# Kernel optimization log

Hardware: AMD Instinct MI355X
Metric: run time of the kernel (lower is better)

The kernel has to match this reference:

```python
import jax, jax.numpy as jnp
import numpy as np

DIM = 1536
NUM_HEADS = 12
HEAD_DIM = DIM // NUM_HEADS  # 128
EPS = 1e-6


def _rms_norm(x, weight, eps=EPS):
    # x: [B, S, C], computed in float32 like the torch module
    xf = x.astype(jnp.float32)
    xf = xf * jax.lax.rsqrt(jnp.mean(xf * xf, axis=-1, keepdims=True) + eps)
    return (xf * weight).astype(x.dtype)


def _rotate_half(x):
    x1, x2 = jnp.split(x, 2, axis=-1)
    return jnp.concatenate([-x2, x1], axis=-1)


def setup_inputs() -> dict:
    key = jax.random.key(0)
    ks = jax.random.split(key, 12)
    B, S = 1, 4096
    scale = 1.0 / np.sqrt(DIM)
    x = jax.random.normal(ks[0], (B, S, DIM), dtype=jnp.float32)
    # RoPE tables [S, head_dim]
    pos = jnp.arange(S, dtype=jnp.float32)[:, None]
    inv_freq = 1.0 / (10000.0 ** (jnp.arange(0, HEAD_DIM, 2, dtype=jnp.float32) / HEAD_DIM))
    ang = pos * inv_freq[None, :]                      # [S, head_dim/2]
    ang = jnp.concatenate([ang, ang], axis=-1)         # [S, head_dim]
    freqs_cos = jnp.cos(ang)
    freqs_sin = jnp.sin(ang)
    Wq = jax.random.normal(ks[1], (DIM, DIM), dtype=jnp.float32) * scale
    bq = jnp.zeros((DIM,), dtype=jnp.float32)
    Wk = jax.random.normal(ks[2], (DIM, DIM), dtype=jnp.float32) * scale
    bk = jnp.zeros((DIM,), dtype=jnp.float32)
    Wv = jax.random.normal(ks[3], (DIM, DIM), dtype=jnp.float32) * scale
    bv = jnp.zeros((DIM,), dtype=jnp.float32)
    Wo = jax.random.normal(ks[4], (DIM, DIM), dtype=jnp.float32) * scale
    bo = jnp.zeros((DIM,), dtype=jnp.float32)
    gq = jnp.ones((DIM,), dtype=jnp.float32)
    gk = jnp.ones((DIM,), dtype=jnp.float32)
    return {"x": x, "freqs_cos": freqs_cos, "freqs_sin": freqs_sin,
            "Wq": Wq, "bq": bq, "Wk": Wk, "bk": bk, "Wv": Wv, "bv": bv,
            "Wo": Wo, "bo": bo, "gq": gq, "gk": gk}


def reference(x, freqs_cos, freqs_sin, Wq, bq, Wk, bk, Wv, bv, Wo, bo, gq, gk):
    b, s, _ = x.shape
    n, d = NUM_HEADS, HEAD_DIM
    q = _rms_norm(x @ Wq.T + bq, gq).reshape(b, s, n, d)
    k = _rms_norm(x @ Wk.T + bk, gk).reshape(b, s, n, d)
    v = (x @ Wv.T + bv).reshape(b, s, n, d)
    # RoPE: freqs [S, d] -> broadcast over batch and heads
    cos = freqs_cos[None, :, None, :]
    sin = freqs_sin[None, :, None, :]
    q = q * cos + _rotate_half(q) * sin
    k = k * cos + _rotate_half(k) * sin
    # SDPA, non-causal
    scores = jnp.einsum('bqnd,bknd->bnqk', q, k) / jnp.sqrt(jnp.asarray(d, x.dtype))
    attn = jax.nn.softmax(scores, axis=-1)
    out = jnp.einsum('bnqk,bknd->bqnd', attn, v).reshape(b, s, n * d)
    return out @ Wo.T + bo
```

## Files before the change

### kernel.cpp

```cpp
#include <hip/hip_runtime.h>

typedef unsigned short ushort_t;
typedef short bf16x8 __attribute__((ext_vector_type(8)));
typedef float f32x4 __attribute__((ext_vector_type(4)));
typedef float f32x16 __attribute__((ext_vector_type(16)));

#define S_LEN 4096
#define DIM   1536
#define NH    12
#define HD    128

__device__ __forceinline__ float bf2f(ushort_t h) {
  union { unsigned u; float f; } v; v.u = ((unsigned)h) << 16; return v.f;
}
__device__ __forceinline__ ushort_t f2bf(float f) {
  union { float f; unsigned u; } v; v.f = f;
  return (ushort_t)((v.u + 0x7FFFu + ((v.u >> 16) & 1u)) >> 16);
}
__device__ __forceinline__ unsigned cvtpk(float lo, float hi_) {
  unsigned r; asm("v_cvt_pk_bf16_f32 %0, %1, %2" : "=v"(r) : "v"(lo), "v"(hi_)); return r;
}

#define GLD16(gp, lp) __builtin_amdgcn_global_load_lds( \
    (const __attribute__((address_space(1))) unsigned int*)(gp), \
    (__attribute__((address_space(3))) unsigned int*)(lp), 16, 0, 0)

__global__ void __launch_bounds__(256) cvt_bf16(const float* __restrict__ in,
                                                ushort_t* __restrict__ out, int n4) {
  int i = blockIdx.x * 256 + threadIdx.x;
  int stride = gridDim.x * 256;
  for (; i < n4; i += stride) {
    float4 v = ((const float4*)in)[i];
    ushort4 o;
    o.x = f2bf(v.x); o.y = f2bf(v.y); o.z = f2bf(v.z); o.w = f2bf(v.w);
    ((ushort4*)out)[i] = o;
  }
}

template <int F32OUT>
__global__ void __launch_bounds__(256) gemm_bt(
    const ushort_t* __restrict__ A, const ushort_t* __restrict__ Wbase,
    const float* __restrict__ b0, const float* __restrict__ b1, const float* __restrict__ b2,
    void* __restrict__ Cbase_v, int M, int N, int K)
{
  const int z = blockIdx.z;
  const ushort_t* W = Wbase + (size_t)z * N * K;
  const float* bias = (z == 0) ? b0 : (z == 1) ? b1 : b2;

  const int n0 = blockIdx.x * 128;
  const int m0 = blockIdx.y * 128;
  const int t = threadIdx.x;
  const int lane = t & 63;
  const int w = t >> 6;
  const int wr = w >> 1, wc = w & 1;
  const int mp = lane & 15, g = lane >> 4;

  __shared__ __attribute__((aligned(16))) ushort_t As[128 * 64];
  __shared__ __attribute__((aligned(16))) ushort_t Bs[128 * 64];

  f32x4 acc[4][4];
  f32x4 zero = {0.f, 0.f, 0.f, 0.f};
#pragma unroll
  for (int i = 0; i < 4; ++i)
#pragma unroll
    for (int j = 0; j < 4; ++j) acc[i][j] = zero;

  for (int kt = 0; kt < K; kt += 64) {
    __syncthreads();
#pragma unroll
    for (int i = 0; i < 4; ++i) {
      int p = i * 256 + t;
      int r = p >> 3, sl = p & 7;
      int sg = sl ^ (r & 7);
      GLD16(A + (size_t)(m0 + r) * K + kt + sg * 8, As + p * 8);
      GLD16(W + (size_t)(n0 + r) * K + kt + sg * 8, Bs + p * 8);
    }
    __syncthreads();
#pragma unroll
    for (int kk = 0; kk < 2; ++kk) {
      bf16x8 af[4], bfr[4];
#pragma unroll
      for (int mi = 0; mi < 4; ++mi) {
        int row = wr * 64 + mi * 16 + mp;
        int ch = (g + 4 * kk) ^ (row & 7);
        af[mi] = *(const bf16x8*)(As + row * 64 + ch * 8);
      }
#pragma unroll
      for (int ni = 0; ni < 4; ++ni) {
        int row = wc * 64 + ni * 16 + mp;
        int ch = (g + 4 * kk) ^ (row & 7);
        bfr[ni] = *(const bf16x8*)(Bs + row * 64 + ch * 8);
      }
#pragma unroll
      for (int mi = 0; mi < 4; ++mi)
#pragma unroll
        for (int ni = 0; ni < 4; ++ni)
          acc[mi][ni] = __builtin_amdgcn_mfma_f32_16x16x32_bf16(af[mi], bfr[ni], acc[mi][ni], 0, 0, 0);
    }
  }
#pragma unroll
  for (int ni = 0; ni < 4; ++ni) {
    int n = n0 + wc * 64 + ni * 16 + mp;
    float bv = bias[n];
#pragma unroll
    for (int mi = 0; mi < 4; ++mi) {
      int mbase = m0 + wr * 64 + mi * 16 + g * 4;
#pragma unroll
      for (int j = 0; j < 4; ++j) {
        if constexpr (F32OUT) {
          ((float*)Cbase_v)[(size_t)z * M * N + (size_t)(mbase + j) * N + n] =
              acc[mi][ni][j] + bv;
        } else {
          ((ushort_t*)Cbase_v)[(size_t)z * M * N + (size_t)(mbase + j) * N + n] =
              f2bf(acc[mi][ni][j] + bv);
        }
      }
    }
  }
}

__global__ void __launch_bounds__(256) epi_qkv(
    const ushort_t* __restrict__ raw,
    const float* __restrict__ gq, const float* __restrict__ gk,
    const float* __restrict__ fcos, const float* __restrict__ fsin,
    ushort_t* __restrict__ Qh, ushort_t* __restrict__ Kh, ushort_t* __restrict__ Vh)
{
  const int s = blockIdx.x;
  const int t = threadIdx.x;
  const ushort_t* rq = raw + (size_t)s * DIM;
  const ushort_t* rk = raw + (size_t)S_LEN * DIM + (size_t)s * DIM;
  const ushort_t* rv = raw + 2 * (size_t)S_LEN * DIM + (size_t)s * DIM;

  float sq = 0.f, sk = 0.f;
#pragma unroll
  for (int i = 0; i < 6; ++i) {
    int e = t + 256 * i;
    float a = bf2f(rq[e]); sq += a * a;
    float b = bf2f(rk[e]); sk += b * b;
  }
  for (int off = 1; off < 64; off <<= 1) {
    sq += __shfl_xor(sq, off, 64);
    sk += __shfl_xor(sk, off, 64);
  }
  __shared__ float red[2][4];
  int w = t >> 6;
  if ((t & 63) == 0) { red[0][w] = sq; red[1][w] = sk; }
  __syncthreads();
  sq = red[0][0] + red[0][1] + red[0][2] + red[0][3];
  sk = red[1][0] + red[1][1] + red[1][2] + red[1][3];
  float invq = rsqrtf(sq * (1.f / 1536.f) + 1e-6f);
  float invk = rsqrtf(sk * (1.f / 1536.f) + 1e-6f);

  const float qscale = 0.12752004708465604f;
#pragma unroll
  for (int i = 0; i < 3; ++i) {
    int p = t + 256 * i;
    int hh = p >> 6, d = p & 63;
    int e1 = hh * 128 + d, e2 = e1 + 64;
    float c1 = fcos[s * 128 + d],      s1 = fsin[s * 128 + d];
    float c2 = fcos[s * 128 + d + 64], s2 = fsin[s * 128 + d + 64];
    float q1 = bf2f(rq[e1]) * invq * gq[e1];
    float q2 = bf2f(rq[e2]) * invq * gq[e2];
    float k1 = bf2f(rk[e1]) * invk * gk[e1];
    float k2 = bf2f(rk[e2]) * invk * gk[e2];
    size_t ob = ((size_t)hh * S_LEN + s) * 128;
    Qh[ob + d]      = f2bf((q1 * c1 - q2 * s1) * qscale);
    Qh[ob + d + 64] = f2bf((q2 * c2 + q1 * s2) * qscale);
    Kh[ob + d]      = f2bf(k1 * c1 - k2 * s1);
    Kh[ob + d + 64] = f2bf(k2 * c2 + k1 * s2);
  }
#pragma unroll
  for (int i = 0; i < 6; ++i) {
    int e = t + 256 * i;
    int hh = e >> 7, d = e & 127;
    Vh[((size_t)hh * S_LEN + s) * 128 + d] = rv[e];
  }
}

__global__ void __launch_bounds__(256) transpose_v(const ushort_t* __restrict__ Vh,
                                                   ushort_t* __restrict__ VT) {
  const int st = blockIdx.x * 64;
  const int dt = blockIdx.y * 64;
  const int h = blockIdx.z;
  __shared__ ushort_t tile[64][65];
  const int t = threadIdx.x;
#pragma unroll
  for (int i = 0; i < 2; ++i) {
    int p = i * 256 + t;
    int r = p >> 3, c = (p & 7) * 8;
    bf16x8 v = *(const bf16x8*)(Vh + ((size_t)h * S_LEN + st + r) * 128 + dt + c);
#pragma unroll
    for (int j = 0; j < 8; ++j) tile[r][c + j] = ((ushort_t*)&v)[j];
  }
  __syncthreads();
#pragma unroll
  for (int i = 0; i < 2; ++i) {
    int p = i * 256 + t;
    int r = p >> 3, c = (p & 7) * 8;
    ushort_t tmp[8];
#pragma unroll
    for (int j = 0; j < 8; ++j) tmp[j] = tile[c + j][r];
    *(bf16x8*)(VT + ((size_t)h * 128 + dt + r) * S_LEN + st + c) = *(bf16x8*)tmp;
  }
}

__global__ void __launch_bounds__(128) attn32(
    const ushort_t* __restrict__ Qh, const ushort_t* __restrict__ Kh,
    const ushort_t* __restrict__ VT, ushort_t* __restrict__ hb)
{
  const int qt = blockIdx.x;
  const int h = blockIdx.y;
  const int t = threadIdx.x;
  const int lane = t & 63;
  const int w = t >> 6;
  const int ql = lane & 31;
  const int hi = lane >> 5;

  __shared__ __attribute__((aligned(16))) ushort_t Ks[64 * 128];
  __shared__ __attribute__((aligned(16))) ushort_t Vs[128 * 64];

  const int q0 = qt * 64 + w * 32;
  const size_t kbase = (size_t)h * S_LEN * 128;
  const size_t vbase = (size_t)h * 128 * S_LEN;

  bf16x8 qf[8];
#pragma unroll
  for (int s = 0; s < 8; ++s)
    qf[s] = *(const bf16x8*)(Qh + ((size_t)h * S_LEN + q0 + ql) * 128 + 16 * s + 8 * hi);

  f32x16 oacc[4];
#pragma unroll
  for (int dt = 0; dt < 4; ++dt)
#pragma unroll
    for (int r = 0; r < 16; ++r) oacc[dt][r] = 0.f;
  float mrun = -1e30f, lrun = 0.f;

  for (int kv0 = 0; kv0 < S_LEN; kv0 += 64) {
    __syncthreads();
#pragma unroll
    for (int i = 0; i < 8; ++i) {
      int p = i * 128 + t;
      int r = p >> 4, sl = p & 15;
      int sg = sl ^ (r & 7);
      GLD16(Kh + kbase + (size_t)(kv0 + r) * 128 + sg * 8, Ks + p * 8);
    }
#pragma unroll
    for (int i = 0; i < 8; ++i) {
      int p = i * 128 + t;
      int r = p >> 3, sl = p & 7;
      int sg = sl ^ (r & 7);
      GLD16(VT + vbase + (size_t)r * S_LEN + kv0 + sg * 8, Vs + p * 8);
    }
    __syncthreads();

    f32x16 sa0, sa1;
#pragma unroll
    for (int r = 0; r < 16; ++r) { sa0[r] = 0.f; sa1[r] = 0.f; }
    __builtin_amdgcn_s_setprio(1);
#pragma unroll
    for (int s = 0; s < 8; ++s) {
      int ck = (2 * s + hi) ^ (ql & 7);
      bf16x8 k0 = *(const bf16x8*)(Ks + ql * 128 + ck * 8);
      bf16x8 k1 = *(const bf16x8*)(Ks + (32 + ql) * 128 + ck * 8);
      sa0 = __builtin_amdgcn_mfma_f32_32x32x16_bf16(k0, qf[s], sa0, 0, 0, 0);
      sa1 = __builtin_amdgcn_mfma_f32_32x32x16_bf16(k1, qf[s], sa1, 0, 0, 0);
    }
    __builtin_amdgcn_s_setprio(0);

    float mt[8];
#pragma unroll
    for (int r = 0; r < 8; ++r)
      mt[r] = fmaxf(fmaxf(sa0[r], sa0[r + 8]), fmaxf(sa1[r], sa1[r + 8]));
#pragma unroll
    for (int off = 4; off > 0; off >>= 1)
#pragma unroll
      for (int r = 0; r < 8; ++r)
        if (r < off) mt[r] = fmaxf(mt[r], mt[r + off]);
    float mx = fmaxf(mt[0], __shfl_xor(mt[0], 32));

    if (__any(mx - mrun > 11.0f)) {
      float nm = fmaxf(mrun, mx);
      float sc = exp2f(mrun - nm);
      mrun = nm;
      lrun *= sc;
#pragma unroll
      for (int dt = 0; dt < 4; ++dt)
#pragma unroll
        for (int r = 0; r < 16; ++r) oacc[dt][r] *= sc;
    }

    float rt[8];
#pragma unroll
    for (int r = 0; r < 16; ++r) {
      sa0[r] = exp2f(sa0[r] - mrun);
      sa1[r] = exp2f(sa1[r] - mrun);
    }
#pragma unroll
    for (int r = 0; r < 8; ++r) rt[r] = (sa0[r] + sa0[r + 8]) + (sa1[r] + sa1[r + 8]);
#pragma unroll
    for (int off = 4; off > 0; off >>= 1)
#pragma unroll
      for (int r = 0; r < 8; ++r)
        if (r < off) rt[r] += rt[r + off];
    lrun += rt[0] + __shfl_xor(rt[0], 32);

    unsigned pw0[8], pw1[8];
#pragma unroll
    for (int a = 0; a < 4; ++a) {
      pw0[2 * a]     = cvtpk(sa0[4 * a], sa0[4 * a + 1]);
      pw0[2 * a + 1] = cvtpk(sa0[4 * a + 2], sa0[4 * a + 3]);
      pw1[2 * a]     = cvtpk(sa1[4 * a], sa1[4 * a + 1]);
      pw1[2 * a + 1] = cvtpk(sa1[4 * a + 2], sa1[4 * a + 3]);
    }

#pragma unroll
    for (int st = 0; st < 2; ++st) {
#pragma unroll
      for (int ks = 0; ks < 2; ++ks) {
        unsigned q0w0 = st ? pw1[4 * ks + 0] : pw0[4 * ks + 0];
        unsigned q0w1 = st ? pw1[4 * ks + 1] : pw0[4 * ks + 1];
        unsigned q1w0 = st ? pw1[4 * ks + 2] : pw0[4 * ks + 2];
        unsigned q1w1 = st ? pw1[4 * ks + 3] : pw0[4 * ks + 3];
        unsigned sw0 = hi ? q0w0 : q1w0;
        unsigned sw1 = hi ? q0w1 : q1w1;
        unsigned rv0 = (unsigned)__shfl_xor((int)sw0, 32);
        unsigned rv1 = (unsigned)__shfl_xor((int)sw1, 32);
        union { unsigned u[4]; bf16x8 v; } fw;
        fw.u[0] = hi ? rv0 : q0w0;
        fw.u[1] = hi ? rv1 : q0w1;
        fw.u[2] = hi ? q1w0 : rv0;
        fw.u[3] = hi ? q1w1 : rv1;
        __builtin_amdgcn_s_setprio(1);
#pragma unroll
        for (int dt = 0; dt < 4; ++dt) {
          int d = 32 * dt + ql;
          int cv = (4 * st + 2 * ks + hi) ^ (ql & 7);
          bf16x8 va = *(const bf16x8*)(Vs + d * 64 + cv * 8);
          oacc[dt] = __builtin_amdgcn_mfma_f32_32x32x16_bf16(va, fw.v, oacc[dt], 0, 0, 0);
        }
        __builtin_amdgcn_s_setprio(0);
      }
    }
  }

  float inv = 1.f / lrun;
#pragma unroll
  for (int dt = 0; dt < 4; ++dt) {
#pragma unroll
    for (int c = 0; c < 4; ++c) {
      float f0 = oacc[dt][4 * c + 0] * inv, f1 = oacc[dt][4 * c + 1] * inv;
      float f2 = oacc[dt][4 * c + 2] * inv, f3 = oacc[dt][4 * c + 3] * inv;
      uint2 u;
      u.x = cvtpk(f0, f1);
      u.y = cvtpk(f2, f3);
      *(uint2*)(hb + (size_t)(q0 + ql) * DIM + h * 128 + 32 * dt + 8 * c + 4 * hi) = u;
    }
  }
}

extern "C" void kernel_launch(void* const* d_in, const int* in_sizes, int n_in,
                              void* d_out, int out_size, void* d_ws, size_t ws_size,
                              hipStream_t stream) {
  const float* x    = (const float*)d_in[0];
  const float* fcos = (const float*)d_in[1];
  const float* fsin = (const float*)d_in[2];
  const float* Wq   = (const float*)d_in[3];
  const float* bq   = (const float*)d_in[4];
  const float* Wk   = (const float*)d_in[5];
  const float* bk   = (const float*)d_in[6];
  const float* Wv   = (const float*)d_in[7];
  const float* bv   = (const float*)d_in[8];
  const float* Wo   = (const float*)d_in[9];
  const float* bo   = (const float*)d_in[10];
  const float* gq   = (const float*)d_in[11];
  const float* gk   = (const float*)d_in[12];

  char* ws = (char*)d_ws;
  ushort_t* xb  = (ushort_t*)(ws);
  ushort_t* wb  = (ushort_t*)(ws + 12582912);
  ushort_t* raw = (ushort_t*)(ws + 31457280);
  ushort_t* Qh  = (ushort_t*)(ws + 69206016);
  ushort_t* Kh  = (ushort_t*)(ws + 81788928);
  ushort_t* Vh  = (ushort_t*)(ws + 94371840);
  ushort_t* VT  = (ushort_t*)(ws + 106954752);
  ushort_t* hb  = (ushort_t*)(ws + 119537664);

  cvt_bf16<<<2048, 256, 0, stream>>>(x,  xb,             6291456 / 4);
  cvt_bf16<<<2048, 256, 0, stream>>>(Wq, wb + 0 * 2359296, 2359296 / 4);
  cvt_bf16<<<2048, 256, 0, stream>>>(Wk, wb + 1 * 2359296, 2359296 / 4);
  cvt_bf16<<<2048, 256, 0, stream>>>(Wv, wb + 2 * 2359296, 2359296 / 4);
  cvt_bf16<<<2048, 256, 0, stream>>>(Wo, wb + 3 * 2359296, 2359296 / 4);

  gemm_bt<0><<<dim3(12, 32, 3), 256, 0, stream>>>(xb, wb, bq, bk, bv,
                                                  (void*)raw, 4096, 1536, 1536);
  epi_qkv<<<4096, 256, 0, stream>>>(raw, gq, gk, fcos, fsin, Qh, Kh, Vh);
  transpose_v<<<dim3(64, 2, 12), 256, 0, stream>>>(Vh, VT);
  attn32<<<dim3(64, 12), 128, 0, stream>>>(Qh, Kh, VT, hb);
  gemm_bt<1><<<dim3(12, 32, 1), 256, 0, stream>>>(hb, wb + 3 * 2359296, bo, bo, bo,
                                                  (void*)d_out, 4096, 1536, 1536);
}
```

Baseline: 577.3 us.

## Split attention over KV into four partitions with a log-sum-exp combine kernel

```diff
diff --git a/kernel.cpp b/kernel.cpp
--- a/kernel.cpp
+++ b/kernel.cpp
@@ -9,6 +9,9 @@
 #define DIM   1536
 #define NH    12
 #define HD    128
+#define KVSPLIT 4
+#define ROWS (NH * S_LEN)
+#define OPSPLIT_ELEMS ((size_t)ROWS * HD)
 
 __device__ __forceinline__ float bf2f(ushort_t h) {
   union { unsigned u; float f; } v; v.u = ((unsigned)h) << 16; return v.f;
@@ -206,10 +209,13 @@
 
 __global__ void __launch_bounds__(128) attn32(
     const ushort_t* __restrict__ Qh, const ushort_t* __restrict__ Kh,
-    const ushort_t* __restrict__ VT, ushort_t* __restrict__ hb)
+    const ushort_t* __restrict__ VT,
+    ushort_t* __restrict__ opraw, ushort_t* __restrict__ opxb,
+    float* __restrict__ mlbuf)
 {
   const int qt = blockIdx.x;
   const int h = blockIdx.y;
+  const int z = blockIdx.z;
   const int t = threadIdx.x;
   const int lane = t & 63;
   const int w = t >> 6;
@@ -235,7 +241,9 @@
     for (int r = 0; r < 16; ++r) oacc[dt][r] = 0.f;
   float mrun = -1e30f, lrun = 0.f;
 
-  for (int kv0 = 0; kv0 < S_LEN; kv0 += 64) {
+  const int kvbeg = z * (S_LEN / KVSPLIT);
+  const int kvend = kvbeg + S_LEN / KVSPLIT;
+  for (int kv0 = kvbeg; kv0 < kvend; kv0 += 64) {
     __syncthreads();
 #pragma unroll
     for (int i = 0; i < 8; ++i) {
@@ -343,6 +351,8 @@
     }
   }
 
+  ushort_t* Op = (z < 3) ? (opraw + (size_t)z * OPSPLIT_ELEMS) : opxb;
+  const int row = h * S_LEN + q0 + ql;
   float inv = 1.f / lrun;
 #pragma unroll
   for (int dt = 0; dt < 4; ++dt) {
@@ -353,9 +363,55 @@
       uint2 u;
       u.x = cvtpk(f0, f1);
       u.y = cvtpk(f2, f3);
-      *(uint2*)(hb + (size_t)(q0 + ql) * DIM + h * 128 + 32 * dt + 8 * c + 4 * hi) = u;
-    }
-  }
+      *(uint2*)(Op + (size_t)row * 128 + 32 * dt + 8 * c + 4 * hi) = u;
+    }
+  }
+  if (hi == 0) {
+    mlbuf[2 * ((size_t)z * ROWS + row)]     = mrun;
+    mlbuf[2 * ((size_t)z * ROWS + row) + 1] = lrun;
+  }
+}
+
+__global__ void __launch_bounds__(256) attn_combine(
+    const ushort_t* __restrict__ opraw, const ushort_t* __restrict__ opxb,
+    const float* __restrict__ mlbuf, ushort_t* __restrict__ hb)
+{
+  int gidx = blockIdx.x * 256 + threadIdx.x;
+  int r = gidx >> 4;
+  int c = gidx & 15;
+
+  float m[KVSPLIT], l[KVSPLIT];
+#pragma unroll
+  for (int zz = 0; zz < KVSPLIT; ++zz) {
+    m[zz] = mlbuf[2 * ((size_t)zz * ROWS + r)];
+    l[zz] = mlbuf[2 * ((size_t)zz * ROWS + r) + 1];
+  }
+  float M = fmaxf(fmaxf(m[0], m[1]), fmaxf(m[2], m[3]));
+  float wsum = 0.f, wz[KVSPLIT];
+#pragma unroll
+  for (int zz = 0; zz < KVSPLIT; ++zz) {
+    wz[zz] = l[zz] * exp2f(m[zz] - M);
+    wsum += wz[zz];
+  }
+  float invw = 1.f / wsum;
+
+  float o[8];
+#pragma unroll
+  for (int j = 0; j < 8; ++j) o[j] = 0.f;
+#pragma unroll
+  for (int zz = 0; zz < KVSPLIT; ++zz) {
+    const ushort_t* Op = (zz < 3) ? (opraw + (size_t)zz * OPSPLIT_ELEMS) : opxb;
+    bf16x8 v = *(const bf16x8*)(Op + (size_t)r * 128 + c * 8);
+#pragma unroll
+    for (int j = 0; j < 8; ++j) o[j] += wz[zz] * bf2f((ushort_t)v[j]);
+  }
+  uint4 u;
+  u.x = cvtpk(o[0] * invw, o[1] * invw);
+  u.y = cvtpk(o[2] * invw, o[3] * invw);
+  u.z = cvtpk(o[4] * invw, o[5] * invw);
+  u.w = cvtpk(o[6] * invw, o[7] * invw);
+  int q = r & (S_LEN - 1), h = r >> 12;
+  *(uint4*)(hb + (size_t)q * DIM + h * 128 + c * 8) = u;
 }
 
 extern "C" void kernel_launch(void* const* d_in, const int* in_sizes, int n_in,
@@ -395,7 +451,8 @@
                                                   (void*)raw, 4096, 1536, 1536);
   epi_qkv<<<4096, 256, 0, stream>>>(raw, gq, gk, fcos, fsin, Qh, Kh, Vh);
   transpose_v<<<dim3(64, 2, 12), 256, 0, stream>>>(Vh, VT);
-  attn32<<<dim3(64, 12), 128, 0, stream>>>(Qh, Kh, VT, hb);
+  attn32<<<dim3(64, 12, KVSPLIT), 128, 0, stream>>>(Qh, Kh, VT, raw, xb, (float*)Vh);
+  attn_combine<<<3072, 256, 0, stream>>>(raw, xb, (const float*)Vh, hb);
   gemm_bt<1><<<dim3(12, 32, 1), 256, 0, stream>>>(hb, wb + 3 * 2359296, bo, bo, bo,
                                                   (void*)d_out, 4096, 1536, 1536);
 }
```

After: 529.7 us. 8.2% less time.
